# Optimization experiments

Hardware: AMD Instinct MI355X
Metric: run time of the kernel (lower is better)

The kernel has to match this reference:

```python
import jax, jax.numpy as jnp
import numpy as np
import math

B, L, D, DFF, H, NL = 32, 512, 1024, 4096, 16, 4
DH = D // H


def setup_inputs() -> dict:
    key = jax.random.key(0)
    ks = jax.random.split(key, 12)
    s = 0.02
    f32 = jnp.float32
    inp = {
        "x_a": jax.random.normal(ks[0], (B, L, D), f32),
        "x_b": jax.random.normal(ks[1], (B, L, D), f32),
        "speaker_emb": jax.random.normal(ks[2], (B, 1, D), f32),
        "Wq": jax.random.normal(ks[3], (NL, D, D), f32) * s,
        "bq": jnp.zeros((NL, D), f32),
        "Wk": jax.random.normal(ks[4], (NL, D, D), f32) * s,
        "bk": jnp.zeros((NL, D), f32),
        "Wv": jax.random.normal(ks[5], (NL, D, D), f32) * s,
        "bv": jnp.zeros((NL, D), f32),
        "Wo": jax.random.normal(ks[6], (NL, D, D), f32) * s,
        "bo": jnp.zeros((NL, D), f32),
        "ln_g": jnp.ones((NL, D), f32),
        "ln_b": jnp.zeros((NL, D), f32),
        "ffn_ln_g": jnp.ones((NL, D), f32),
        "ffn_ln_b": jnp.zeros((NL, D), f32),
        "W1": jax.random.normal(ks[7], (NL, D, DFF), f32) * s,
        "b1": jnp.zeros((NL, DFF), f32),
        "W2": jax.random.normal(ks[8], (NL, DFF, D), f32) * s,
        "b2": jnp.zeros((NL, D), f32),
    }
    return inp


def _gelu(x):
    # tanh-approx gelu, exactly as in the torch source
    c = math.sqrt(2.0 / math.pi)
    return 0.5 * x * (1.0 + jnp.tanh(c * (x + 0.044715 * x * x * x)))


def _ln(x, g, b, eps=1e-6):
    mu = jnp.mean(x, axis=-1, keepdims=True)
    var = jnp.mean(jnp.square(x - mu), axis=-1, keepdims=True)
    return (x - mu) * jax.lax.rsqrt(var + eps) * g + b


def _pos_encoding(seq_len, dim):
    pos = np.arange(seq_len)[:, None].astype(np.float32)
    div = np.exp(np.arange(0, dim, 2, dtype=np.float32) * (-math.log(10000.0) / dim))
    pe = np.zeros((seq_len, dim), dtype=np.float32)
    pe[:, 0::2] = np.sin(pos * div)
    pe[:, 1::2] = np.cos(pos * div)
    return jnp.asarray(pe)[None]  # [1, L, D]


def _forward(x_a, x_b, speaker_emb, Wq, bq, Wk, bk, Wv, bv, Wo, bo,
             ln_g, ln_b, ffn_ln_g, ffn_ln_b, W1, b1, W2, b2):
    pe = _pos_encoding(x_a.shape[1], x_a.shape[2])
    # cross branch: x_a != x_b. dropout is eval-mode identity.
    x_a = x_a + pe + speaker_emb
    x_b = x_b + pe + speaker_emb
    n_layers = Wq.shape[0]
    scale = 1.0 / math.sqrt(DH)
    for i in range(n_layers):
        xb_n = _ln(x_b, ln_g[i], ln_b[i]) if i != 0 else x_b
        # MHA: key=x_a, value=x_a, query=xb_n
        q = (xb_n @ Wq[i] + bq[i]).reshape(B, -1, H, DH)
        k = (x_a @ Wk[i] + bk[i]).reshape(B, -1, H, DH)
        v = (x_a @ Wv[i] + bv[i]).reshape(B, -1, H, DH)
        scores = jnp.einsum("bqhd,bkhd->bhqk", q * scale, k)
        attn = jax.nn.softmax(scores, axis=-1)
        ctx = jnp.einsum("bhqk,bkhd->bqhd", attn, v).reshape(B, -1, D)
        context = ctx @ Wo[i] + bo[i]
        out = context + xb_n  # residual onto (possibly normed) inputs_b
        # PositionwiseFeedForward (pre-LN, gelu, residual)
        inter = _gelu(_ln(out, ffn_ln_g[i], ffn_ln_b[i]) @ W1[i] + b1[i])
        x_b = inter @ W2[i] + b2[i] + out
    return x_b


def reference(x_a, x_b, speaker_emb, Wq, bq, Wk, bk, Wv, bv, Wo, bo,
              ln_g, ln_b, ffn_ln_g, ffn_ln_b, W1, b1, W2, b2):
    return _forward(x_a, x_b, speaker_emb, Wq, bq, Wk, bk, Wv, bv, Wo, bo,
                    ln_g, ln_b, ffn_ln_g, ffn_ln_b, W1, b1, W2, b2)
```

## Files before the change

kernel.cpp:

```cpp
#include <hip/hip_runtime.h>

#define BATCH 32
#define SEQ   512
#define DMOD  1024
#define DFFN  4096
#define NHEAD 16
#define DHEAD 64
#define NLAY  4
#define NTOK  (BATCH * SEQ)

typedef __attribute__((ext_vector_type(8))) short short8;
typedef __attribute__((ext_vector_type(4))) float f32x4;
typedef unsigned int uint32;

__device__ __forceinline__ unsigned short f2bf(float f) {
  uint32 u = __builtin_bit_cast(uint32, f);
  u += 0x7fffu + ((u >> 16) & 1u);
  return (unsigned short)(u >> 16);
}
__device__ __forceinline__ float gelu_f(float x) {
  float u = 0.7978845608028654f * (x + 0.044715f * x * x * x);
  u = fminf(fmaxf(u, -15.f), 15.f);
  float e = __expf(2.f * u);
  return 0.5f * x * (1.f + (e - 1.f) / (e + 1.f));
}

#define GLOAD16(g, l) __builtin_amdgcn_global_load_lds( \
    (const __attribute__((address_space(1))) void*)(g), \
    (__attribute__((address_space(3))) void*)(l), 16, 0, 0)

#define MFMA16(a, b, c) __builtin_amdgcn_mfma_f32_16x16x32_bf16((a), (b), (c), 0, 0, 0)

__global__ __launch_bounds__(256) void pe_kernel(float* __restrict__ pe) {
  const int idx = blockIdx.x * 256 + threadIdx.x;
  const int l = idx >> 9;
  const int i = idx & 511;
  const float dv = __expf((float)(2 * i) * (-9.210340371976184f / (float)DMOD));
  const float a = (float)l * dv;
  pe[(size_t)l * DMOD + 2 * i]     = sinf(a);
  pe[(size_t)l * DMOD + 2 * i + 1] = cosf(a);
}

__global__ __launch_bounds__(256) void prep_kernel(
    const float* __restrict__ xa, const float* __restrict__ xb,
    const float* __restrict__ pe, const float* __restrict__ spk,
    float* __restrict__ xb32, unsigned short* __restrict__ oa16,
    unsigned short* __restrict__ ob16)
{
  const int z = blockIdx.z;
  const float* x = z ? xb : xa;
  unsigned short* o16 = z ? ob16 : oa16;
  const size_t id4 = (size_t)blockIdx.x * 256 + threadIdx.x;
  const size_t e = id4 * 4;
  const int b  = (int)(e >> 19);
  const int ld = (int)(e & ((1u << 19) - 1));
  const int d  = (int)(e & 1023);
  float4 xv = ((const float4*)x)[id4];
  float4 pv = ((const float4*)pe)[ld >> 2];
  float4 sv = ((const float4*)spk)[(size_t)b * 256 + (d >> 2)];
  float4 o;
  o.x = xv.x + pv.x + sv.x;
  o.y = xv.y + pv.y + sv.y;
  o.z = xv.z + pv.z + sv.z;
  o.w = xv.w + pv.w + sv.w;
  if (z) ((float4*)xb32)[id4] = o;
  ushort4 h;
  h.x = f2bf(o.x); h.y = f2bf(o.y); h.z = f2bf(o.z); h.w = f2bf(o.w);
  ((ushort4*)o16)[id4] = h;
}

__global__ __launch_bounds__(256) void wtrans_all(
    const float* __restrict__ Wq, const float* __restrict__ Wk,
    const float* __restrict__ Wv, const float* __restrict__ Wo,
    const float* __restrict__ W1, const float* __restrict__ W2, int layer,
    unsigned short* __restrict__ Wqt, unsigned short* __restrict__ Wkt,
    unsigned short* __restrict__ Wvt, unsigned short* __restrict__ Wot,
    unsigned short* __restrict__ W1t, unsigned short* __restrict__ W2t)
{
  __shared__ float tile[64][65];
  const int bid = blockIdx.x;
  const float* W; unsigned short* Wt; int K, N, bx, by;
  if (bid < 1024) {
    const int which = bid >> 8, r = bid & 255;
    bx = r & 15; by = r >> 4; K = DMOD; N = DMOD;
    const size_t off = (size_t)layer * DMOD * DMOD;
    W  = (which == 0 ? Wq : which == 1 ? Wk : which == 2 ? Wv : Wo) + off;
    Wt = (which == 0 ? Wqt : which == 1 ? Wkt : which == 2 ? Wvt : Wot);
  } else if (bid < 2048) {
    const int r = bid - 1024;
    bx = r & 63; by = r >> 6; K = DMOD; N = DFFN;
    W = W1 + (size_t)layer * DMOD * DFFN; Wt = W1t;
  } else {
    const int r = bid - 2048;
    bx = r & 15; by = r >> 4; K = DFFN; N = DMOD;
    W = W2 + (size_t)layer * DMOD * DFFN; Wt = W2t;
  }
  const int n0 = bx * 64, k0 = by * 64;
  const int tx = threadIdx.x & 63, ty = threadIdx.x >> 6;
  #pragma unroll
  for (int i = 0; i < 16; i++) {
    int r = ty + 4 * i;
    tile[r][tx] = W[(size_t)(k0 + r) * N + n0 + tx];
  }
  __syncthreads();
  #pragma unroll
  for (int i = 0; i < 16; i++) {
    int rn = ty + 4 * i;
    Wt[(size_t)(n0 + rn) * K + k0 + tx] = f2bf(tile[tx][rn]);
  }
}

template<int WRITE_F32>
__global__ __launch_bounds__(256) void ln_kernel(
    const float* __restrict__ x, const float* __restrict__ g, const float* __restrict__ bta,
    float* __restrict__ of32, unsigned short* __restrict__ o16)
{
  const int row = blockIdx.x;
  const int t = threadIdx.x;
  const float4 v = ((const float4*)(x + (size_t)row * DMOD))[t];
  float s  = v.x + v.y + v.z + v.w;
  float s2 = v.x*v.x + v.y*v.y + v.z*v.z + v.w*v.w;
  #pragma unroll
  for (int off = 32; off > 0; off >>= 1) {
    s  += __shfl_down(s, off);
    s2 += __shfl_down(s2, off);
  }
  __shared__ float red[8];
  if ((t & 63) == 0) { red[(t >> 6) * 2] = s; red[(t >> 6) * 2 + 1] = s2; }
  __syncthreads();
  const float sum  = red[0] + red[2] + red[4] + red[6];
  const float sum2 = red[1] + red[3] + red[5] + red[7];
  const float mean = sum * (1.f / (float)DMOD);
  const float var  = sum2 * (1.f / (float)DMOD) - mean * mean;
  const float rstd = rsqrtf(var + 1e-6f);
  const float4 gg = ((const float4*)g)[t];
  const float4 bb = ((const float4*)bta)[t];
  float4 o;
  o.x = (v.x - mean) * rstd * gg.x + bb.x;
  o.y = (v.y - mean) * rstd * gg.y + bb.y;
  o.z = (v.z - mean) * rstd * gg.z + bb.z;
  o.w = (v.w - mean) * rstd * gg.w + bb.w;
  if (WRITE_F32) ((float4*)of32)[(size_t)row * 256 + t] = o;
  ushort4 h;
  h.x = f2bf(o.x); h.y = f2bf(o.y); h.z = f2bf(o.z); h.w = f2bf(o.w);
  ((ushort4*)o16)[(size_t)row * 256 + t] = h;
}

template<int MODE>
__global__ __launch_bounds__(512, 4) void gemm128(
    const unsigned short* __restrict__ A0, const unsigned short* __restrict__ A1,
    const unsigned short* __restrict__ B0, const unsigned short* __restrict__ B1,
    const unsigned short* __restrict__ B2,
    const float* __restrict__ bias0, const float* __restrict__ bias1,
    const float* __restrict__ bias2, const float* __restrict__ res,
    void* out0, void* out1, void* out2, int N, int K)
{
  __shared__ unsigned short Sh[32768];
  unsigned short* As = Sh;
  unsigned short* Bs = Sh + 8192;
  const int t = threadIdx.x;
  const int lane = t & 63, w = t >> 6;
  const int wm = w >> 2, wn = w & 3;
  const int g = lane >> 4, rm = lane & 15;

  const int gx = gridDim.x, gy = gridDim.y;
  const int nwg = gx * gy * gridDim.z;
  const int hid = (blockIdx.z * gy + blockIdx.y) * gx + blockIdx.x;
  const int wid = (hid & 7) * (nwg >> 3) + (hid >> 3);
  const int bx = wid % gx;
  const int rest = wid / gx;
  const int by = rest % gy;
  const int z  = rest / gy;

  const unsigned short* A  = (MODE == 0 && z) ? A1 : A0;
  const unsigned short* Bt = (MODE == 0) ? (z == 0 ? B0 : z == 1 ? B1 : B2) : B0;
  const float* bias        = (MODE == 0) ? (z == 0 ? bias0 : z == 1 ? bias1 : bias2) : bias0;
  void* outp               = (MODE == 0) ? (z == 0 ? out0 : z == 1 ? out1 : out2) : out0;

  const size_t tm = (size_t)by * 128;
  const size_t tn = (size_t)bx * 256;

  const int ia0 = t, ia1 = 512 + t;
  const int ra0 = ia0 >> 3, ra1 = ia1 >> 3;
  const int ca0 = 8 * ((ia0 & 7) ^ (ra0 & 7));
  const int ca1 = 8 * ((ia1 & 7) ^ (ra1 & 7));
  const int ib0 = t, ib1 = 512 + t, ib2 = 1024 + t, ib3 = 1536 + t;
  const int rb0 = ib0 >> 3, rb1 = ib1 >> 3, rb2 = ib2 >> 3, rb3 = ib3 >> 3;
  const int cb0 = 8 * ((ib0 & 7) ^ (rb0 & 7));
  const int cb1 = 8 * ((ib1 & 7) ^ (rb1 & 7));
  const int cb2 = 8 * ((ib2 & 7) ^ (rb2 & 7));
  const int cb3 = 8 * ((ib3 & 7) ^ (rb3 & 7));
  const unsigned short* Ab0 = A + (tm + ra0) * (size_t)K + ca0;
  const unsigned short* Ab1 = A + (tm + ra1) * (size_t)K + ca1;
  const unsigned short* Bb0 = Bt + (tn + rb0) * (size_t)K + cb0;
  const unsigned short* Bb1 = Bt + (tn + rb1) * (size_t)K + cb1;
  const unsigned short* Bb2 = Bt + (tn + rb2) * (size_t)K + cb2;
  const unsigned short* Bb3 = Bt + (tn + rb3) * (size_t)K + cb3;

  int aoff[4], boff[4];
  #pragma unroll
  for (int fm = 0; fm < 4; fm++) {
    const int r = wm * 64 + fm * 16 + rm;
    aoff[fm] = r * 128 + ((g ^ (r & 7)) * 16);
  }
  #pragma unroll
  for (int fn = 0; fn < 4; fn++) {
    const int r = wn * 64 + fn * 16 + rm;
    boff[fn] = r * 128 + ((g ^ (r & 7)) * 16);
  }

  f32x4 acc[4][4];
  #pragma unroll
  for (int i = 0; i < 4; i++)
    #pragma unroll
    for (int j = 0; j < 4; j++)
      acc[i][j] = (f32x4){0.f, 0.f, 0.f, 0.f};

  const int nt = K >> 6;
  for (int kt = 0; kt < nt; kt++) {
    const int k0 = kt * 64;
    GLOAD16(Ab0 + k0, &As[ia0 * 8]);
    GLOAD16(Ab1 + k0, &As[ia1 * 8]);
    GLOAD16(Bb0 + k0, &Bs[ib0 * 8]);
    GLOAD16(Bb1 + k0, &Bs[ib1 * 8]);
    GLOAD16(Bb2 + k0, &Bs[ib2 * 8]);
    GLOAD16(Bb3 + k0, &Bs[ib3 * 8]);
    __syncthreads();
    {
      short8 a[4], b[4];
      #pragma unroll
      for (int fm = 0; fm < 4; fm++) a[fm] = *(const short8*)((const char*)As + aoff[fm]);
      #pragma unroll
      for (int fn = 0; fn < 4; fn++) b[fn] = *(const short8*)((const char*)Bs + boff[fn]);
      #pragma unroll
      for (int fm = 0; fm < 4; fm++)
        #pragma unroll
        for (int fn = 0; fn < 4; fn++)
          acc[fm][fn] = MFMA16(a[fm], b[fn], acc[fm][fn]);
    }
    {
      short8 a[4], b[4];
      #pragma unroll
      for (int fm = 0; fm < 4; fm++) a[fm] = *(const short8*)((const char*)As + (aoff[fm] ^ 64));
      #pragma unroll
      for (int fn = 0; fn < 4; fn++) b[fn] = *(const short8*)((const char*)Bs + (boff[fn] ^ 64));
      #pragma unroll
      for (int fm = 0; fm < 4; fm++)
        #pragma unroll
        for (int fn = 0; fn < 4; fn++)
          acc[fm][fn] = MFMA16(a[fm], b[fn], acc[fm][fn]);
    }
    __syncthreads();
  }

  if (MODE == 2 || MODE == 3) {
    #pragma unroll
    for (int fn = 0; fn < 4; fn++) {
      const size_t gcol = tn + wn * 64 + fn * 16 + rm;
      const float bc = bias[gcol];
      #pragma unroll
      for (int fm = 0; fm < 4; fm++) {
        #pragma unroll
        for (int r = 0; r < 4; r++) {
          const size_t grow = tm + wm * 64 + fm * 16 + g * 4 + r;
          const size_t off = grow * (size_t)N + gcol;
          float v = acc[fm][fn][r] + bc;
          if (MODE == 2) ((float*)outp)[off] = v + res[off];
          else { float* op = (float*)outp; op[off] = v + op[off]; }
        }
      }
    }
  } else if (MODE == 0) {
    unsigned short* eb = Sh + w * 4096;
    if (z == 2) {
      #pragma unroll
      for (int fn = 0; fn < 4; fn++) {
        const float bc = bias[tn + wn * 64 + fn * 16 + rm];
        #pragma unroll
        for (int fm = 0; fm < 4; fm++)
          #pragma unroll
          for (int r = 0; r < 4; r++) {
            const int tok = fm * 16 + g * 4 + r;
            const int ch  = fn * 16 + rm;
            eb[ch * 64 + (tok ^ ((ch & 7) << 3))] = f2bf(acc[fm][fn][r] + bc);
          }
      }
      const int tok0 = (int)tm + wm * 64;
      const int bb = tok0 >> 9, l0 = tok0 & 511;
      #pragma unroll
      for (int pass = 0; pass < 8; pass++) {
        const int ch = pass * 8 + (lane >> 3);
        const int t8 = (lane & 7) * 8;
        short8 vv = *(const short8*)&eb[ch * 64 + (t8 ^ ((ch & 7) << 3))];
        *(short8*)((unsigned short*)outp +
                   ((size_t)bb * 1024 + tn + wn * 64 + ch) * 512 + l0 + t8) = vv;
      }
    } else {
      #pragma unroll
      for (int fn = 0; fn < 4; fn++) {
        const float bc = bias[tn + wn * 64 + fn * 16 + rm];
        #pragma unroll
        for (int fm = 0; fm < 4; fm++)
          #pragma unroll
          for (int r = 0; r < 4; r++) {
            float v = acc[fm][fn][r] + bc;
            if (z == 0) v *= 0.125f;
            const int lr = fm * 16 + g * 4 + r;
            const int lc = fn * 16 + rm;
            eb[lr * 64 + (lc ^ (g << 4))] = f2bf(v);
          }
      }
      #pragma unroll
      for (int pass = 0; pass < 8; pass++) {
        const int lr = pass * 8 + (lane >> 3);
        const int lc8 = (lane & 7) * 8;
        const int q = (lr >> 2) & 3;
        short8 vv = *(const short8*)&eb[lr * 64 + (lc8 ^ (q << 4))];
        *(short8*)((unsigned short*)outp +
                   (tm + wm * 64 + lr) * (size_t)N + tn + wn * 64 + lc8) = vv;
      }
    }
  } else {
    unsigned short* eb = Sh + w * 4096;
    #pragma unroll
    for (int fn = 0; fn < 4; fn++) {
      const float bc = bias[tn + wn * 64 + fn * 16 + rm];
      #pragma unroll
      for (int fm = 0; fm < 4; fm++)
        #pragma unroll
        for (int r = 0; r < 4; r++) {
          const int lr = fm * 16 + g * 4 + r;
          const int lc = fn * 16 + rm;
          eb[lr * 64 + (lc ^ (g << 4))] = f2bf(gelu_f(acc[fm][fn][r] + bc));
        }
    }
    #pragma unroll
    for (int pass = 0; pass < 8; pass++) {
      const int lr = pass * 8 + (lane >> 3);
      const int lc8 = (lane & 7) * 8;
      const int q = (lr >> 2) & 3;
      short8 vv = *(const short8*)&eb[lr * 64 + (lc8 ^ (q << 4))];
      *(short8*)((unsigned short*)outp +
                 (tm + wm * 64 + lr) * (size_t)N + tn + wn * 64 + lc8) = vv;
    }
  }
}

__global__ __launch_bounds__(256) void attn_mfma(
    const unsigned short* __restrict__ qb, const unsigned short* __restrict__ kb,
    const unsigned short* __restrict__ vt, unsigned short* __restrict__ ctx)
{
  __shared__ unsigned short Sh[8192];
  __shared__ unsigned short Ps[4][32 * 72];
  unsigned short* Ks = Sh;
  unsigned short* Vs = Sh + 4096;
  const int t = threadIdx.x;
  const int lane = t & 63, w = t >> 6;
  const int g = lane >> 4, rm = lane & 15;
  const int qt = blockIdx.x, h = blockIdx.y, b = blockIdx.z;

  const unsigned short* qg = qb + ((size_t)(b * SEQ + qt * 128)) * DMOD + h * DHEAD;
  const unsigned short* kg = kb + ((size_t)(b * SEQ)) * DMOD + h * DHEAD;
  const unsigned short* vg = vt + ((size_t)(b * NHEAD + h)) * DHEAD * SEQ;

  #pragma unroll
  for (int ii = 0; ii < 4; ii++) {
    const int i = ii * 256 + t;
    const int r = i >> 3, c = i & 7;
    const int bc = 16 * (c ^ (r & 7));
    GLOAD16(qg + (size_t)r * DMOD + (bc >> 1), Sh + (size_t)(ii * 256 + w * 64) * 8);
  }
  __syncthreads();

  short8 aq[2][2];
  #pragma unroll
  for (int fq = 0; fq < 2; fq++)
    #pragma unroll
    for (int kd = 0; kd < 2; kd++) {
      const int r = w * 32 + fq * 16 + rm;
      aq[fq][kd] = *(const short8*)((const char*)Sh + r * 128 + ((kd * 64 + g * 16) ^ ((r & 7) << 4)));
    }
  __syncthreads();

  float mrow[2][4], lsum[2][4];
  f32x4 of[2][4];
  #pragma unroll
  for (int fq = 0; fq < 2; fq++) {
    #pragma unroll
    for (int j = 0; j < 4; j++) { mrow[fq][j] = -INFINITY; lsum[fq][j] = 0.f; }
    #pragma unroll
    for (int fd = 0; fd < 4; fd++) of[fq][fd] = (f32x4){0.f, 0.f, 0.f, 0.f};
  }

  for (int kt = 0; kt < SEQ / 64; kt++) {
    {
      const int i = t, r = i >> 3, c = i & 7;
      const int bc = 16 * (c ^ (r & 7));
      GLOAD16(kg + (size_t)(kt * 64 + r) * DMOD + (bc >> 1), Ks + (size_t)w * 512);
    }
    {
      const int i = 256 + t, r = i >> 3, c = i & 7;
      const int bc = 16 * (c ^ (r & 7));
      GLOAD16(kg + (size_t)(kt * 64 + r) * DMOD + (bc >> 1), Ks + 2048 + (size_t)w * 512);
    }
    {
      const int i = t, r = i >> 3, c = i & 7;
      const int bc = 16 * (c ^ (r & 7));
      GLOAD16(vg + (size_t)r * SEQ + kt * 64 + (bc >> 1), Vs + (size_t)w * 512);
    }
    {
      const int i = 256 + t, r = i >> 3, c = i & 7;
      const int bc = 16 * (c ^ (r & 7));
      GLOAD16(vg + (size_t)r * SEQ + kt * 64 + (bc >> 1), Vs + 2048 + (size_t)w * 512);
    }
    __syncthreads();

    f32x4 s[2][4];
    #pragma unroll
    for (int fq = 0; fq < 2; fq++)
      #pragma unroll
      for (int fk = 0; fk < 4; fk++) {
        f32x4 a = (f32x4){0.f, 0.f, 0.f, 0.f};
        #pragma unroll
        for (int kd = 0; kd < 2; kd++) {
          const int r = fk * 16 + rm;
          short8 bk = *(const short8*)((const char*)Ks + r * 128 + ((kd * 64 + g * 16) ^ ((r & 7) << 4)));
          a = MFMA16(aq[fq][kd], bk, a);
        }
        s[fq][fk] = a;
      }

    float pm[2][4];
    int grow = 0;
    #pragma unroll
    for (int fq = 0; fq < 2; fq++)
      #pragma unroll
      for (int j = 0; j < 4; j++) {
        float mx = fmaxf(fmaxf(s[fq][0][j], s[fq][1][j]), fmaxf(s[fq][2][j], s[fq][3][j]));
        #pragma unroll
        for (int mk = 1; mk < 16; mk <<= 1) mx = fmaxf(mx, __shfl_xor(mx, mk));
        pm[fq][j] = mx;
        grow |= (mx > mrow[fq][j] + 8.f);
      }
    if (__any(grow)) {
      #pragma unroll
      for (int fq = 0; fq < 2; fq++)
        #pragma unroll
        for (int j = 0; j < 4; j++) {
          const float mn = fmaxf(mrow[fq][j], pm[fq][j]);
          const float corr = __expf(mrow[fq][j] - mn);
          mrow[fq][j] = mn;
          lsum[fq][j] *= corr;
          #pragma unroll
          for (int fd = 0; fd < 4; fd++) of[fq][fd][j] *= corr;
        }
    }
    #pragma unroll
    for (int fq = 0; fq < 2; fq++)
      #pragma unroll
      for (int j = 0; j < 4; j++) {
        const int prow = (fq * 16 + g * 4 + j) * 72;
        float psum = 0.f;
        #pragma unroll
        for (int fk = 0; fk < 4; fk++) {
          const float p = __expf(s[fq][fk][j] - mrow[fq][j]);
          psum += p;
          Ps[w][prow + fk * 16 + rm] = f2bf(p);
        }
        lsum[fq][j] += psum;
      }

    #pragma unroll
    for (int fq = 0; fq < 2; fq++) {
      short8 pa0 = *(const short8*)&Ps[w][(fq * 16 + rm) * 72 + g * 8];
      short8 pa1 = *(const short8*)&Ps[w][(fq * 16 + rm) * 72 + 32 + g * 8];
      #pragma unroll
      for (int fd = 0; fd < 4; fd++) {
        const int r = fd * 16 + rm;
        const short8 vb0 = *(const short8*)((const char*)Vs + r * 128 + ((g * 16) ^ ((r & 7) << 4)));
        const short8 vb1 = *(const short8*)((const char*)Vs + r * 128 + ((64 + g * 16) ^ ((r & 7) << 4)));
        of[fq][fd] = MFMA16(pa0, vb0, of[fq][fd]);
        of[fq][fd] = MFMA16(pa1, vb1, of[fq][fd]);
      }
    }

    __syncthreads();
  }

  #pragma unroll
  for (int fq = 0; fq < 2; fq++)
    #pragma unroll
    for (int j = 0; j < 4; j++) {
      float ls = lsum[fq][j];
      #pragma unroll
      for (int mk = 1; mk < 16; mk <<= 1) ls += __shfl_xor(ls, mk);
      const float inv = 1.f / ls;
      const size_t q = (size_t)b * SEQ + qt * 128 + w * 32 + fq * 16 + g * 4 + j;
      #pragma unroll
      for (int fd = 0; fd < 4; fd++)
        ctx[q * DMOD + h * DHEAD + fd * 16 + rm] = f2bf(of[fq][fd][j] * inv);
    }
}

extern "C" void kernel_launch(void* const* d_in, const int* in_sizes, int n_in,
                              void* d_out, int out_size, void* d_ws, size_t ws_size,
                              hipStream_t stream) {
  const float* x_a   = (const float*)d_in[0];
  const float* x_b   = (const float*)d_in[1];
  const float* spk   = (const float*)d_in[2];
  const float* Wq    = (const float*)d_in[3];
  const float* bq    = (const float*)d_in[4];
  const float* Wk    = (const float*)d_in[5];
  const float* bk    = (const float*)d_in[6];
  const float* Wv    = (const float*)d_in[7];
  const float* bv    = (const float*)d_in[8];
  const float* Wo    = (const float*)d_in[9];
  const float* bo    = (const float*)d_in[10];
  const float* ln_g  = (const float*)d_in[11];
  const float* ln_b  = (const float*)d_in[12];
  const float* fln_g = (const float*)d_in[13];
  const float* fln_b = (const float*)d_in[14];
  const float* W1    = (const float*)d_in[15];
  const float* b1    = (const float*)d_in[16];
  const float* W2    = (const float*)d_in[17];
  const float* b2    = (const float*)d_in[18];
  float* out = (float*)d_out;

  char* ws = (char*)d_ws;
  size_t o = 0;
  auto give = [&](size_t bytes) { char* p = ws + o; o += (bytes + 255) & ~(size_t)255; return p; };
  const size_t ACT2 = (size_t)NTOK * DMOD * 2;

  unsigned short* qb16  = (unsigned short*)give(ACT2);
  unsigned short* kb16  = (unsigned short*)give(ACT2);
  unsigned short* vt16  = (unsigned short*)give(ACT2);
  unsigned short* ctx16 = (unsigned short*)give(ACT2);
  unsigned short* xa16  = (unsigned short*)give(ACT2);
  unsigned short* xbn16 = (unsigned short*)give(ACT2);
  float*          outf  = (float*)give((size_t)NTOK * DMOD * 4);
  unsigned short* Wqt   = (unsigned short*)give((size_t)DMOD * DMOD * 2);
  unsigned short* Wkt   = (unsigned short*)give((size_t)DMOD * DMOD * 2);
  unsigned short* Wvt   = (unsigned short*)give((size_t)DMOD * DMOD * 2);
  unsigned short* Wot   = (unsigned short*)give((size_t)DMOD * DMOD * 2);
  unsigned short* W1t   = (unsigned short*)give((size_t)DMOD * DFFN * 2);
  unsigned short* W2t   = (unsigned short*)give((size_t)DMOD * DFFN * 2);
  float*          peb   = (float*)give((size_t)SEQ * DMOD * 4);
  unsigned short* inter = qb16;
  (void)ws_size; (void)in_sizes; (void)n_in; (void)out_size;

  const dim3 blk(256);
  const dim3 blk512(512);

  pe_kernel<<<dim3((SEQ * (DMOD / 2)) / 256), blk, 0, stream>>>(peb);
  const int nprep = (NTOK * DMOD / 4) / 256;
  prep_kernel<<<dim3(nprep, 1, 2), blk, 0, stream>>>(x_a, x_b, peb, spk, out, xa16, xbn16);

  const dim3 gQKV(DMOD / 256, NTOK / 128, 3);
  const dim3 gWO (DMOD / 256, NTOK / 128);
  const dim3 gW1 (DFFN / 256, NTOK / 128);
  const dim3 gW2 (DMOD / 256, NTOK / 128);

  for (int i = 0; i < NLAY; i++) {
    wtrans_all<<<dim3(3072), blk, 0, stream>>>(Wq, Wk, Wv, Wo, W1, W2, i,
                                               Wqt, Wkt, Wvt, Wot, W1t, W2t);
    if (i != 0) {
      ln_kernel<1><<<dim3(NTOK), blk, 0, stream>>>(out, ln_g + (size_t)i * DMOD, ln_b + (size_t)i * DMOD, outf, xbn16);
    }
    gemm128<0><<<gQKV, blk512, 0, stream>>>(
        xbn16, xa16, Wqt, Wkt, Wvt,
        bq + (size_t)i * DMOD, bk + (size_t)i * DMOD, bv + (size_t)i * DMOD,
        nullptr, qb16, kb16, vt16, DMOD, DMOD);
    attn_mfma<<<dim3(SEQ / 128, NHEAD, BATCH), blk, 0, stream>>>(qb16, kb16, vt16, ctx16);
    if (i == 0) {
      gemm128<2><<<gWO, blk512, 0, stream>>>(
          ctx16, nullptr, Wot, nullptr, nullptr,
          bo + (size_t)i * DMOD, nullptr, nullptr, out, outf, nullptr, nullptr, DMOD, DMOD);
    } else {
      gemm128<3><<<gWO, blk512, 0, stream>>>(
          ctx16, nullptr, Wot, nullptr, nullptr,
          bo + (size_t)i * DMOD, nullptr, nullptr, nullptr, outf, nullptr, nullptr, DMOD, DMOD);
    }
    ln_kernel<0><<<dim3(NTOK), blk, 0, stream>>>(outf, fln_g + (size_t)i * DMOD, fln_b + (size_t)i * DMOD, nullptr, xbn16);
    gemm128<1><<<gW1, blk512, 0, stream>>>(
        xbn16, nullptr, W1t, nullptr, nullptr,
        b1 + (size_t)i * DFFN, nullptr, nullptr, nullptr, inter, nullptr, nullptr, DFFN, DMOD);
    gemm128<2><<<gW2, blk512, 0, stream>>>(
        inter, nullptr, W2t, nullptr, nullptr,
        b2 + (size_t)i * DMOD, nullptr, nullptr, outf, out, nullptr, nullptr, DMOD, DFFN);
  }
}
```

Measured before the change: 2.628 ms.

## Keep residual stream in bf16 and drop fp32 intermediate buffer

Replaces the fp32 residual buffer with bf16 storage. Two pieces move with it: the Wo GEMM epilogue adds its result into the bf16 normed input in place (new MODE 4, staged through LDS for vectorized stores), and the W2 GEMM reads a bf16 residual (MODE 5). The prep and LN kernels no longer write fp32 copies, and the FFN LN reads bf16 input. This cuts fp32 activation traffic, and it risks precision loss from rounding the residual to bf16 between stages.

```diff
diff --git a/kernel.cpp b/kernel.cpp
--- a/kernel.cpp
+++ b/kernel.cpp
@@ -18,6 +18,9 @@
   u += 0x7fffu + ((u >> 16) & 1u);
   return (unsigned short)(u >> 16);
 }
+__device__ __forceinline__ float bf2f(unsigned short u) {
+  return __builtin_bit_cast(float, (uint32)u << 16);
+}
 __device__ __forceinline__ float gelu_f(float x) {
   float u = 0.7978845608028654f * (x + 0.044715f * x * x * x);
   u = fminf(fmaxf(u, -15.f), 15.f);
@@ -44,8 +47,7 @@
 __global__ __launch_bounds__(256) void prep_kernel(
     const float* __restrict__ xa, const float* __restrict__ xb,
     const float* __restrict__ pe, const float* __restrict__ spk,
-    float* __restrict__ xb32, unsigned short* __restrict__ oa16,
-    unsigned short* __restrict__ ob16)
+    unsigned short* __restrict__ oa16, unsigned short* __restrict__ ob16)
 {
   const int z = blockIdx.z;
   const float* x = z ? xb : xa;
@@ -58,14 +60,11 @@
   float4 xv = ((const float4*)x)[id4];
   float4 pv = ((const float4*)pe)[ld >> 2];
   float4 sv = ((const float4*)spk)[(size_t)b * 256 + (d >> 2)];
-  float4 o;
-  o.x = xv.x + pv.x + sv.x;
-  o.y = xv.y + pv.y + sv.y;
-  o.z = xv.z + pv.z + sv.z;
-  o.w = xv.w + pv.w + sv.w;
-  if (z) ((float4*)xb32)[id4] = o;
   ushort4 h;
-  h.x = f2bf(o.x); h.y = f2bf(o.y); h.z = f2bf(o.z); h.w = f2bf(o.w);
+  h.x = f2bf(xv.x + pv.x + sv.x);
+  h.y = f2bf(xv.y + pv.y + sv.y);
+  h.z = f2bf(xv.z + pv.z + sv.z);
+  h.w = f2bf(xv.w + pv.w + sv.w);
   ((ushort4*)o16)[id4] = h;
 }
 
@@ -110,14 +109,20 @@
   }
 }
 
-template<int WRITE_F32>
+template<int BF16IN>
 __global__ __launch_bounds__(256) void ln_kernel(
-    const float* __restrict__ x, const float* __restrict__ g, const float* __restrict__ bta,
-    float* __restrict__ of32, unsigned short* __restrict__ o16)
+    const void* __restrict__ xin, const float* __restrict__ g,
+    const float* __restrict__ bta, unsigned short* __restrict__ o16)
 {
   const int row = blockIdx.x;
   const int t = threadIdx.x;
-  const float4 v = ((const float4*)(x + (size_t)row * DMOD))[t];
+  float4 v;
+  if (BF16IN) {
+    ushort4 u = ((const ushort4*)((const unsigned short*)xin + (size_t)row * DMOD))[t];
+    v.x = bf2f(u.x); v.y = bf2f(u.y); v.z = bf2f(u.z); v.w = bf2f(u.w);
+  } else {
+    v = ((const float4*)((const float*)xin + (size_t)row * DMOD))[t];
+  }
   float s  = v.x + v.y + v.z + v.w;
   float s2 = v.x*v.x + v.y*v.y + v.z*v.z + v.w*v.w;
   #pragma unroll
@@ -135,14 +140,11 @@
   const float rstd = rsqrtf(var + 1e-6f);
   const float4 gg = ((const float4*)g)[t];
   const float4 bb = ((const float4*)bta)[t];
-  float4 o;
-  o.x = (v.x - mean) * rstd * gg.x + bb.x;
-  o.y = (v.y - mean) * rstd * gg.y + bb.y;
-  o.z = (v.z - mean) * rstd * gg.z + bb.z;
-  o.w = (v.w - mean) * rstd * gg.w + bb.w;
-  if (WRITE_F32) ((float4*)of32)[(size_t)row * 256 + t] = o;
   ushort4 h;
-  h.x = f2bf(o.x); h.y = f2bf(o.y); h.z = f2bf(o.z); h.w = f2bf(o.w);
+  h.x = f2bf((v.x - mean) * rstd * gg.x + bb.x);
+  h.y = f2bf((v.y - mean) * rstd * gg.y + bb.y);
+  h.z = f2bf((v.z - mean) * rstd * gg.z + bb.z);
+  h.w = f2bf((v.w - mean) * rstd * gg.w + bb.w);
   ((ushort4*)o16)[(size_t)row * 256 + t] = h;
 }
 
@@ -152,7 +154,7 @@
     const unsigned short* __restrict__ B0, const unsigned short* __restrict__ B1,
     const unsigned short* __restrict__ B2,
     const float* __restrict__ bias0, const float* __restrict__ bias1,
-    const float* __restrict__ bias2, const float* __restrict__ res,
+    const float* __restrict__ bias2, const void* __restrict__ resv,
     void* out0, void* out1, void* out2, int N, int K)
 {
   __shared__ unsigned short Sh[32768];
@@ -253,7 +255,8 @@
     __syncthreads();
   }
 
-  if (MODE == 2 || MODE == 3) {
+  if (MODE == 5) {
+    const unsigned short* res16 = (const unsigned short*)resv;
     #pragma unroll
     for (int fn = 0; fn < 4; fn++) {
       const size_t gcol = tn + wn * 64 + fn * 16 + rm;
@@ -264,11 +267,38 @@
         for (int r = 0; r < 4; r++) {
           const size_t grow = tm + wm * 64 + fm * 16 + g * 4 + r;
           const size_t off = grow * (size_t)N + gcol;
-          float v = acc[fm][fn][r] + bc;
-          if (MODE == 2) ((float*)outp)[off] = v + res[off];
-          else { float* op = (float*)outp; op[off] = v + op[off]; }
+          ((float*)outp)[off] = acc[fm][fn][r] + bc + bf2f(res16[off]);
         }
       }
+    }
+  } else if (MODE == 4) {
+    unsigned short* eb = Sh + w * 4096;
+    #pragma unroll
+    for (int fn = 0; fn < 4; fn++) {
+      const float bc = bias[tn + wn * 64 + fn * 16 + rm];
+      #pragma unroll
+      for (int fm = 0; fm < 4; fm++)
+        #pragma unroll
+        for (int r = 0; r < 4; r++) {
+          const int lr = fm * 16 + g * 4 + r;
+          const int lc = fn * 16 + rm;
+          eb[lr * 64 + (lc ^ (g << 4))] = f2bf(acc[fm][fn][r] + bc);
+        }
+    }
+    #pragma unroll
+    for (int pass = 0; pass < 8; pass++) {
+      const int lr = pass * 8 + (lane >> 3);
+      const int lc8 = (lane & 7) * 8;
+      const int q = (lr >> 2) & 3;
+      short8 nv = *(const short8*)&eb[lr * 64 + (lc8 ^ (q << 4))];
+      unsigned short* gp = (unsigned short*)outp +
+                           (tm + wm * 64 + lr) * (size_t)N + tn + wn * 64 + lc8;
+      short8 ov = *(const short8*)gp;
+      short8 rv;
+      #pragma unroll
+      for (int j = 0; j < 8; j++)
+        rv[j] = (short)f2bf(bf2f((unsigned short)nv[j]) + bf2f((unsigned short)ov[j]));
+      *(short8*)gp = rv;
     }
   } else if (MODE == 0) {
     unsigned short* eb = Sh + w * 4096;
@@ -537,7 +567,7 @@
   unsigned short* ctx16 = (unsigned short*)give(ACT2);
   unsigned short* xa16  = (unsigned short*)give(ACT2);
   unsigned short* xbn16 = (unsigned short*)give(ACT2);
-  float*          outf  = (float*)give((size_t)NTOK * DMOD * 4);
+  unsigned short* xn2   = (unsigned short*)give(ACT2);
   unsigned short* Wqt   = (unsigned short*)give((size_t)DMOD * DMOD * 2);
   unsigned short* Wkt   = (unsigned short*)give((size_t)DMOD * DMOD * 2);
   unsigned short* Wvt   = (unsigned short*)give((size_t)DMOD * DMOD * 2);
@@ -553,7 +583,7 @@
 
   pe_kernel<<<dim3((SEQ * (DMOD / 2)) / 256), blk, 0, stream>>>(peb);
   const int nprep = (NTOK * DMOD / 4) / 256;
-  prep_kernel<<<dim3(nprep, 1, 2), blk, 0, stream>>>(x_a, x_b, peb, spk, out, xa16, xbn16);
+  prep_kernel<<<dim3(nprep, 1, 2), blk, 0, stream>>>(x_a, x_b, peb, spk, xa16, xbn16);
 
   const dim3 gQKV(DMOD / 256, NTOK / 128, 3);
   const dim3 gWO (DMOD / 256, NTOK / 128);
@@ -564,28 +594,22 @@
     wtrans_all<<<dim3(3072), blk, 0, stream>>>(Wq, Wk, Wv, Wo, W1, W2, i,
                                                Wqt, Wkt, Wvt, Wot, W1t, W2t);
     if (i != 0) {
-      ln_kernel<1><<<dim3(NTOK), blk, 0, stream>>>(out, ln_g + (size_t)i * DMOD, ln_b + (size_t)i * DMOD, outf, xbn16);
+      ln_kernel<0><<<dim3(NTOK), blk, 0, stream>>>(out, ln_g + (size_t)i * DMOD, ln_b + (size_t)i * DMOD, xbn16);
     }
     gemm128<0><<<gQKV, blk512, 0, stream>>>(
         xbn16, xa16, Wqt, Wkt, Wvt,
         bq + (size_t)i * DMOD, bk + (size_t)i * DMOD, bv + (size_t)i * DMOD,
         nullptr, qb16, kb16, vt16, DMOD, DMOD);
     attn_mfma<<<dim3(SEQ / 128, NHEAD, BATCH), blk, 0, stream>>>(qb16, kb16, vt16, ctx16);
-    if (i == 0) {
-      gemm128<2><<<gWO, blk512, 0, stream>>>(
-          ctx16, nullptr, Wot, nullptr, nullptr,
-          bo + (size_t)i * DMOD, nullptr, nullptr, out, outf, nullptr, nullptr, DMOD, DMOD);
-    } else {
-      gemm128<3><<<gWO, blk512, 0, stream>>>(
-          ctx16, nullptr, Wot, nullptr, nullptr,
-          bo + (size_t)i * DMOD, nullptr, nullptr, nullptr, outf, nullptr, nullptr, DMOD, DMOD);
-    }
-    ln_kernel<0><<<dim3(NTOK), blk, 0, stream>>>(outf, fln_g + (size_t)i * DMOD, fln_b + (size_t)i * DMOD, nullptr, xbn16);
+    gemm128<4><<<gWO, blk512, 0, stream>>>(
+        ctx16, nullptr, Wot, nullptr, nullptr,
+        bo + (size_t)i * DMOD, nullptr, nullptr, nullptr, xbn16, nullptr, nullptr, DMOD, DMOD);
+    ln_kernel<1><<<dim3(NTOK), blk, 0, stream>>>(xbn16, fln_g + (size_t)i * DMOD, fln_b + (size_t)i * DMOD, xn2);
     gemm128<1><<<gW1, blk512, 0, stream>>>(
-        xbn16, nullptr, W1t, nullptr, nullptr,
+        xn2, nullptr, W1t, nullptr, nullptr,
         b1 + (size_t)i * DFFN, nullptr, nullptr, nullptr, inter, nullptr, nullptr, DFFN, DMOD);
-    gemm128<2><<<gW2, blk512, 0, stream>>>(
+    gemm128<5><<<gW2, blk512, 0, stream>>>(
         inter, nullptr, W2t, nullptr, nullptr,
-        b2 + (size_t)i * DMOD, nullptr, nullptr, outf, out, nullptr, nullptr, DMOD, DFFN);
-  }
-}
+        b2 + (size_t)i * DMOD, nullptr, nullptr, xbn16, out, nullptr, nullptr, DMOD, DFFN);
+  }
+}
```

Result: faster. 2.342 ms (-10.9%).
